# Kernel tuning notes

Measured on AMD Instinct MI355X. Metric: run time of the kernel, lower is better.

Reference implementation:

```python
import jax, jax.numpy as jnp
import numpy as np

N, E = 50000, 800000
IN, OUT, H, B = 512, 512, 8, 4  # num_bases=4, aggregators=['symnorm'] (PyG EGConv defaults)
FH = OUT // H  # per-head dim = 64
EPS = 1e-5


def setup_inputs() -> dict:
    key = jax.random.key(0)
    ks = jax.random.split(key, 8)
    s_in = 1.0 / np.sqrt(IN)
    return {
        "x": jax.random.normal(ks[0], (N, IN), jnp.float32),
        "edge_index": jax.random.randint(ks[1], (2, E), 0, N, jnp.int32),
        "W_bases": jax.random.normal(ks[2], (IN, B * FH), jnp.float32) * s_in,  # bases_lin (no bias)
        "W_comb": jax.random.normal(ks[3], (IN, H * B), jnp.float32) * s_in,    # comb_lin weight
        "b_comb": jnp.zeros((H * B,), jnp.float32),                               # comb_lin bias
        "conv_bias": jnp.zeros((OUT,), jnp.float32),                              # EGConv output bias
        "W_res": jax.random.normal(ks[4], (IN, OUT), jnp.float32) * s_in,        # res_connection
        "b_res": jnp.zeros((OUT,), jnp.float32),
        "gamma": jnp.ones((OUT,), jnp.float32),                                   # LayerNorm weight
        "beta": jnp.zeros((OUT,), jnp.float32),                                   # LayerNorm bias
    }


def reference(x, edge_index, W_bases, W_comb, b_comb, conv_bias, W_res, b_res, gamma, beta):
    n = x.shape[0]
    # --- gcn_norm with self-loops (symnorm aggregator) ---
    loops = jnp.arange(n, dtype=edge_index.dtype)
    src = jnp.concatenate([edge_index[0], loops])  # [E+N]
    dst = jnp.concatenate([edge_index[1], loops])
    deg = jax.ops.segment_sum(jnp.ones_like(src, dtype=x.dtype), dst, num_segments=n)
    dinv = jnp.where(deg > 0, jax.lax.rsqrt(jnp.maximum(deg, 1.0)), 0.0)
    norm = dinv[src] * dinv[dst]  # [E+N]

    # --- EGConv: bases projection, symnorm aggregation, per-head combination ---
    bases = x @ W_bases  # [N, B*FH]
    agg = jax.ops.segment_sum(bases[src] * norm[:, None], dst, num_segments=n)  # [N, B*FH]
    weightings = (x @ W_comb + b_comb).reshape(n, H, B)        # [N, H, B]  (num_aggrs=1)
    agg = agg.reshape(n, B, FH)                                  # [N, B, FH]
    conv_out = jnp.einsum('nhb,nbf->nhf', weightings, agg).reshape(n, OUT) + conv_bias

    # --- residual + LayerNorm + ReLU (dropout p=0 -> identity) ---
    out = conv_out + x @ W_res + b_res
    mu = out.mean(-1, keepdims=True)
    var = out.var(-1, keepdims=True)
    out = (out - mu) * jax.lax.rsqrt(var + EPS) * gamma + beta
    return jax.nn.relu(out)
```

## Files before the change

kernel.cpp:

```cpp
#include <hip/hip_runtime.h>
#include <hip/hip_bf16.h>

#define KDIM 512
#define ODIM 512
#define NB 4
#define NH 8
#define FH 64
#define BFH 256
#define HB 32
#define NCAT 896
#define COL_W 256
#define COL_R 288
#define LN_EPS 1e-5f
#define SCAN_BLK 1024

typedef __attribute__((ext_vector_type(8))) short short8;
typedef __attribute__((ext_vector_type(4))) float floatx4;

__device__ __forceinline__ float b2f(unsigned short u) {
    union { unsigned int i; float f; } v; v.i = ((unsigned int)u) << 16; return v.f;
}
__device__ __forceinline__ unsigned short f2b(float f) {
    __hip_bfloat16 h = __float2bfloat16(f);
    return *(unsigned short*)&h;
}
__device__ __forceinline__ void async16(const void* g, void* l) {
    __builtin_amdgcn_global_load_lds(
        (__attribute__((address_space(1))) unsigned int*)(g),
        (__attribute__((address_space(3))) unsigned int*)(l),
        16, 0, 0);
}

__global__ void deg_kernel(const int* __restrict__ dst, int* __restrict__ deg, int E) {
    int i = blockIdx.x * blockDim.x + threadIdx.x;
    if (i < E) atomicAdd(&deg[dst[i]], 1);
}

__global__ __launch_bounds__(256) void scan_sums_kernel(
        const int* __restrict__ deg, int* __restrict__ sums, int N) {
    int t = threadIdx.x;
    int idx = blockIdx.x * SCAN_BLK + t * 4;
    int4 v = {0, 0, 0, 0};
    if (idx + 3 < N) v = *(const int4*)(deg + idx);
    else {
        if (idx < N)     v.x = deg[idx];
        if (idx + 1 < N) v.y = deg[idx + 1];
        if (idx + 2 < N) v.z = deg[idx + 2];
        if (idx + 3 < N) v.w = deg[idx + 3];
    }
    int s = v.x + v.y + v.z + v.w;
    #pragma unroll
    for (int o = 32; o > 0; o >>= 1) s += __shfl_down(s, o, 64);
    __shared__ int ws[4];
    int lane = t & 63, w = t >> 6;
    if (lane == 0) ws[w] = s;
    __syncthreads();
    if (t == 0) sums[blockIdx.x] = ws[0] + ws[1] + ws[2] + ws[3];
}

__global__ __launch_bounds__(1024) void scan_base_kernel(
        int* __restrict__ sums, int nb) {
    __shared__ int sm[1024];
    int t = threadIdx.x;
    int own = (t < nb) ? sums[t] : 0;
    sm[t] = own;
    __syncthreads();
    for (int o = 1; o < 1024; o <<= 1) {
        int u = (t >= o) ? sm[t - o] : 0;
        __syncthreads();
        sm[t] += u;
        __syncthreads();
    }
    if (t < nb) sums[t] = sm[t] - own;
}

__global__ __launch_bounds__(256) void scan_write_kernel(
        const int* __restrict__ deg, const int* __restrict__ bases,
        int* __restrict__ offsets, int* __restrict__ woff,
        float* __restrict__ dinv, int N, int E) {
    int t = threadIdx.x;
    int idx = blockIdx.x * SCAN_BLK + t * 4;
    int4 v = {0, 0, 0, 0};
    if (idx + 3 < N) v = *(const int4*)(deg + idx);
    else {
        if (idx < N)     v.x = deg[idx];
        if (idx + 1 < N) v.y = deg[idx + 1];
        if (idx + 2 < N) v.z = deg[idx + 2];
        if (idx + 3 < N) v.w = deg[idx + 3];
    }
    int s = v.x + v.y + v.z + v.w;
    __shared__ int sm[256];
    sm[t] = s;
    __syncthreads();
    for (int o = 1; o < 256; o <<= 1) {
        int u = (t >= o) ? sm[t - o] : 0;
        __syncthreads();
        sm[t] += u;
        __syncthreads();
    }
    int o0 = sm[t] - s + bases[blockIdx.x];
    int o1 = o0 + v.x, o2 = o1 + v.y, o3 = o2 + v.z;
    if (idx + 3 < N) {
        int4 ov = {o0, o1, o2, o3};
        *(int4*)(offsets + idx) = ov;
        *(int4*)(woff + idx) = ov;
        float4 dv = {rsqrtf((float)v.x + 1.0f), rsqrtf((float)v.y + 1.0f),
                     rsqrtf((float)v.z + 1.0f), rsqrtf((float)v.w + 1.0f)};
        *(float4*)(dinv + idx) = dv;
    } else {
        int oo[4] = {o0, o1, o2, o3};
        int vv[4] = {v.x, v.y, v.z, v.w};
        for (int j = 0; j < 4; j++) {
            if (idx + j < N) {
                offsets[idx + j] = oo[j];
                woff[idx + j] = oo[j];
                dinv[idx + j] = rsqrtf((float)vv[j] + 1.0f);
            }
        }
    }
    if (blockIdx.x == 0 && t == 0) offsets[N] = E;
}

__global__ void fill_kernel(const int* __restrict__ src, const int* __restrict__ dst,
                            int* __restrict__ woff, int* __restrict__ ebuf, int E) {
    int i = blockIdx.x * blockDim.x + threadIdx.x;
    if (i < E) {
        int pos = atomicAdd(&woff[dst[i]], 1);
        ebuf[pos] = src[i];
    }
}

__global__ __launch_bounds__(256) void prep_kernel(
        const float* __restrict__ x, unsigned short* __restrict__ xb, long total4,
        int nCvtBlocks,
        const float* __restrict__ Wb, const float* __restrict__ Wc,
        const float* __restrict__ Wr, const float* __restrict__ bcomb,
        const float* __restrict__ bres,
        unsigned short* __restrict__ wT, float* __restrict__ bias_cat) {
    int blk = blockIdx.x;
    if (blk < nCvtBlocks) {
        long i = (long)blk * 256 + threadIdx.x;
        if (i >= total4) return;
        float4 v = ((const float4*)x)[i];
        ushort4 u;
        u.x = f2b(v.x); u.y = f2b(v.y); u.z = f2b(v.z); u.w = f2b(v.w);
        ((ushort4*)xb)[i] = u;
    } else {
        int idx = (blk - nCvtBlocks) * 256 + threadIdx.x;
        if (idx >= NCAT * KDIM) return;
        int c = idx >> 9, k = idx & (KDIM - 1);
        float v;
        if (c < BFH)                   v = Wb[(size_t)k * BFH + c];
        else if (c < COL_R)            v = Wc[(size_t)k * HB + (c - COL_W)];
        else if (c < COL_R + ODIM)     v = Wr[(size_t)k * ODIM + (c - COL_R)];
        else                           v = 0.0f;
        wT[(size_t)c * KDIM + k] = f2b(v);
        if (k == 0) {
            float bv = 0.0f;
            if (c >= COL_W && c < COL_R)             bv = bcomb[c - COL_W];
            else if (c >= COL_R && c < COL_R + ODIM) bv = bres[c - COL_R];
            bias_cat[c] = bv;
        }
    }
}

#define BM 128
#define BN 128
#define BK 32
#define SLD 136

__global__ __launch_bounds__(256) void mfma_gemm_kernel(
        const unsigned short* __restrict__ xb,
        const unsigned short* __restrict__ wT,
        const float* __restrict__ bias_cat,
        unsigned short* __restrict__ Cb,
        int N) {
    __shared__ short lds[8192];
    short* As = lds;
    short* Bs = lds + 4096;
    int t = threadIdx.x;
    int l = t & 63, w = t >> 6;
    int wr = w >> 1, wc = w & 1;
    int quad = l >> 4, m = l & 15;
    int row0 = blockIdx.y * BM;
    int col0 = blockIdx.x * BN;

    floatx4 acc[4][4];
    floatx4 zero4 = {0.f, 0.f, 0.f, 0.f};
    #pragma unroll
    for (int i = 0; i < 4; i++)
        #pragma unroll
        for (int j = 0; j < 4; j++) acc[i][j] = zero4;

    int ar0 = row0 + (w << 4) + (l >> 2);
    int ar1 = ar0 + 64;
    int brow = col0 + (w << 4) + (l >> 2);
    int kk = (l & 3) * 8;
    const unsigned short* agp0 = xb + (size_t)min(ar0, N - 1) * KDIM + kk;
    const unsigned short* agp1 = xb + (size_t)min(ar1, N - 1) * KDIM + kk;
    const unsigned short* bgp0 = wT + (size_t)brow * KDIM + kk;
    const unsigned short* bgp1 = bgp0 + (size_t)64 * KDIM;
    short* al0 = As + w * 512;
    short* al1 = As + 2048 + w * 512;
    short* bl0 = Bs + w * 512;
    short* bl1 = Bs + 2048 + w * 512;

    for (int k0 = 0; k0 < KDIM; k0 += BK) {
        __syncthreads();
        async16(agp0 + k0, al0);
        async16(agp1 + k0, al1);
        async16(bgp0 + k0, bl0);
        async16(bgp1 + k0, bl1);
        __syncthreads();

        short8 a[4], b[4];
        #pragma unroll
        for (int i = 0; i < 4; i++)
            a[i] = *(const short8*)(As + (wr * 64 + i * 16 + m) * BK + quad * 8);
        #pragma unroll
        for (int j = 0; j < 4; j++)
            b[j] = *(const short8*)(Bs + (wc * 64 + j * 16 + m) * BK + quad * 8);
        #pragma unroll
        for (int i = 0; i < 4; i++)
            #pragma unroll
            for (int j = 0; j < 4; j++)
                acc[i][j] = __builtin_amdgcn_mfma_f32_16x16x32_bf16(
                    a[i], b[j], acc[i][j], 0, 0, 0);
    }

    float bj[4];
    #pragma unroll
    for (int j = 0; j < 4; j++) bj[j] = bias_cat[col0 + wc * 64 + j * 16 + m];

    unsigned short* stage = (unsigned short*)lds;
    #pragma unroll
    for (int i = 0; i < 4; i++) {
        __syncthreads();
        #pragma unroll
        for (int j = 0; j < 4; j++)
            #pragma unroll
            for (int r = 0; r < 4; r++)
                stage[(wr * 16 + quad * 4 + r) * SLD + wc * 64 + j * 16 + m] =
                    f2b(acc[i][j][r] + bj[j]);
        __syncthreads();
        #pragma unroll
        for (int u = t; u < 512; u += 256) {
            int lr = u >> 4, c8 = u & 15;
            int gr = row0 + ((lr & 16) ? 64 : 0) + i * 16 + (lr & 15);
            if (gr < N) {
                int4 v = *(const int4*)(stage + lr * SLD + c8 * 8);
                *(int4*)(Cb + (size_t)gr * NCAT + col0 + c8 * 8) = v;
            }
        }
    }
}

__global__ __launch_bounds__(256) void gather_kernel(
        const int* __restrict__ offsets, const int* __restrict__ ebuf,
        const float* __restrict__ dinv, const unsigned short* __restrict__ Cb,
        unsigned short* __restrict__ agg, int N) {
    int wave = (blockIdx.x * blockDim.x + threadIdx.x) >> 6;
    int lane = threadIdx.x & 63;
    if (wave >= N) return;
    int n = wave;
    float di = dinv[n];
    float self = di * di;
    ushort4 u = ((const ushort4*)(Cb + (size_t)n * NCAT))[lane];
    float ax = b2f(u.x) * self, ay = b2f(u.y) * self;
    float az = b2f(u.z) * self, aw = b2f(u.w) * self;
    int e = offsets[n], end = offsets[n + 1];
    for (; e + 1 < end; e += 2) {
        int s0 = ebuf[e], s1 = ebuf[e + 1];
        float n0 = dinv[s0] * di, n1 = dinv[s1] * di;
        ushort4 u0 = ((const ushort4*)(Cb + (size_t)s0 * NCAT))[lane];
        ushort4 u1 = ((const ushort4*)(Cb + (size_t)s1 * NCAT))[lane];
        ax += b2f(u0.x) * n0 + b2f(u1.x) * n1;
        ay += b2f(u0.y) * n0 + b2f(u1.y) * n1;
        az += b2f(u0.z) * n0 + b2f(u1.z) * n1;
        aw += b2f(u0.w) * n0 + b2f(u1.w) * n1;
    }
    if (e < end) {
        int s0 = ebuf[e];
        float n0 = dinv[s0] * di;
        ushort4 u0 = ((const ushort4*)(Cb + (size_t)s0 * NCAT))[lane];
        ax += b2f(u0.x) * n0; ay += b2f(u0.y) * n0;
        az += b2f(u0.z) * n0; aw += b2f(u0.w) * n0;
    }
    ushort4 r;
    r.x = f2b(ax); r.y = f2b(ay); r.z = f2b(az); r.w = f2b(aw);
    ((ushort4*)(agg + (size_t)n * BFH))[lane] = r;
}

__global__ __launch_bounds__(256) void combine_kernel(
        const unsigned short* __restrict__ agg, const unsigned short* __restrict__ Cb,
        const float* __restrict__ conv_bias, const float* __restrict__ gamma,
        const float* __restrict__ beta, float* __restrict__ out, int N) {
    int wave = (blockIdx.x * blockDim.x + threadIdx.x) >> 6;
    if (wave >= N) return;
    int lane = threadIdx.x & 63;
    int n = wave;
    int h = lane >> 3;
    int f0 = (lane & 7) * 8;
    int t0 = lane * 8;

    const unsigned short* crow = Cb + (size_t)n * NCAT;
    ushort4 wu = *(const ushort4*)(crow + COL_W + h * 4);
    float w0 = b2f(wu.x), w1 = b2f(wu.y), w2 = b2f(wu.z), w3 = b2f(wu.w);

    const unsigned short* arow = agg + (size_t)n * BFH;
    short8 a0 = *(const short8*)(arow + 0 * FH + f0);
    short8 a1 = *(const short8*)(arow + 1 * FH + f0);
    short8 a2 = *(const short8*)(arow + 2 * FH + f0);
    short8 a3 = *(const short8*)(arow + 3 * FH + f0);

    short8 rv = *(const short8*)(crow + COL_R + t0);

    float4 cb0 = *(const float4*)(conv_bias + t0);
    float4 cb1 = *(const float4*)(conv_bias + t0 + 4);
    float cb[8] = {cb0.x, cb0.y, cb0.z, cb0.w, cb1.x, cb1.y, cb1.z, cb1.w};

    float v[8];
    float s = 0.f, s2 = 0.f;
    #pragma unroll
    for (int j = 0; j < 8; j++) {
        float conv = w0 * b2f((unsigned short)a0[j]) + w1 * b2f((unsigned short)a1[j])
                   + w2 * b2f((unsigned short)a2[j]) + w3 * b2f((unsigned short)a3[j]);
        float val = conv + cb[j] + b2f((unsigned short)rv[j]);
        v[j] = val;
        s += val;
        s2 += val * val;
    }
    #pragma unroll
    for (int o = 32; o > 0; o >>= 1) {
        s  += __shfl_xor(s, o, 64);
        s2 += __shfl_xor(s2, o, 64);
    }
    float mu = s * (1.0f / (float)ODIM);
    float var = s2 * (1.0f / (float)ODIM) - mu * mu;
    float rstd = rsqrtf(var + LN_EPS);

    float4 g0 = *(const float4*)(gamma + t0);
    float4 g1 = *(const float4*)(gamma + t0 + 4);
    float4 be0 = *(const float4*)(beta + t0);
    float4 be1 = *(const float4*)(beta + t0 + 4);
    float g[8] = {g0.x, g0.y, g0.z, g0.w, g1.x, g1.y, g1.z, g1.w};
    float be[8] = {be0.x, be0.y, be0.z, be0.w, be1.x, be1.y, be1.z, be1.w};

    float ov[8];
    #pragma unroll
    for (int j = 0; j < 8; j++) {
        float o = (v[j] - mu) * rstd * g[j] + be[j];
        ov[j] = fmaxf(o, 0.0f);
    }
    float4* op = (float4*)(out + (size_t)n * ODIM + t0);
    op[0] = make_float4(ov[0], ov[1], ov[2], ov[3]);
    op[1] = make_float4(ov[4], ov[5], ov[6], ov[7]);
}

static inline char* ws_alloc(char*& p, size_t bytes) {
    char* r = p;
    p += (bytes + 255) & ~(size_t)255;
    return r;
}

extern "C" void kernel_launch(void* const* d_in, const int* in_sizes, int n_in,
                              void* d_out, int out_size, void* d_ws, size_t ws_size,
                              hipStream_t stream) {
    const float* x         = (const float*)d_in[0];
    const int*   ei        = (const int*)d_in[1];
    const float* W_bases   = (const float*)d_in[2];
    const float* W_comb    = (const float*)d_in[3];
    const float* b_comb    = (const float*)d_in[4];
    const float* conv_bias = (const float*)d_in[5];
    const float* W_res     = (const float*)d_in[6];
    const float* b_res     = (const float*)d_in[7];
    const float* gamma     = (const float*)d_in[8];
    const float* beta      = (const float*)d_in[9];

    int N = in_sizes[0] / KDIM;
    int E = in_sizes[1] / 2;
    const int* src = ei;
    const int* dst = ei + E;
    int nScanBlocks = (N + SCAN_BLK - 1) / SCAN_BLK;

    char* p = (char*)d_ws;
    int*   deg      = (int*)ws_alloc(p, sizeof(int) * (size_t)N);
    int*   offsets  = (int*)ws_alloc(p, sizeof(int) * (size_t)(N + 1));
    int*   woff     = (int*)ws_alloc(p, sizeof(int) * (size_t)N);
    int*   ebuf     = (int*)ws_alloc(p, sizeof(int) * (size_t)E);
    int*   sums     = (int*)ws_alloc(p, sizeof(int) * (size_t)nScanBlocks);
    float* dinv     = (float*)ws_alloc(p, sizeof(float) * (size_t)N);
    float* bias_cat = (float*)ws_alloc(p, sizeof(float) * NCAT);
    unsigned short* agg = (unsigned short*)ws_alloc(p, 2ull * N * BFH);
    unsigned short* Cb  = (unsigned short*)ws_alloc(p, 2ull * N * NCAT);
    unsigned short* xb  = (unsigned short*)ws_alloc(p, 2ull * N * KDIM);
    unsigned short* wT  = (unsigned short*)ws_alloc(p, 2ull * NCAT * KDIM);
    float* out = (float*)d_out;

    hipMemsetAsync(deg, 0, sizeof(int) * (size_t)N, stream);

    long total4 = (long)N * KDIM / 4;
    int nCvtBlocks = (int)((total4 + 255) / 256);
    int nStageBlocks = (NCAT * KDIM + 255) / 256;
    prep_kernel<<<nCvtBlocks + nStageBlocks, 256, 0, stream>>>(
        x, xb, total4, nCvtBlocks, W_bases, W_comb, W_res, b_comb, b_res,
        wT, bias_cat);

    deg_kernel<<<(E + 255) / 256, 256, 0, stream>>>(dst, deg, E);
    scan_sums_kernel<<<nScanBlocks, 256, 0, stream>>>(deg, sums, N);
    scan_base_kernel<<<1, 1024, 0, stream>>>(sums, nScanBlocks);
    scan_write_kernel<<<nScanBlocks, 256, 0, stream>>>(deg, sums, offsets, woff,
                                                       dinv, N, E);
    fill_kernel<<<(E + 255) / 256, 256, 0, stream>>>(src, dst, woff, ebuf, E);

    dim3 gg(NCAT / BN, (N + BM - 1) / BM);
    mfma_gemm_kernel<<<gg, 256, 0, stream>>>(xb, wT, bias_cat, Cb, N);

    gather_kernel<<<(N + 3) / 4, 256, 0, stream>>>(offsets, ebuf, dinv, Cb, agg, N);
    combine_kernel<<<(N + 3) / 4, 256, 0, stream>>>(agg, Cb, conv_bias, gamma,
                                                    beta, out, N);
}
```

Baseline: 467.9 us.

## Double-buffer GEMM LDS tiles and remap workgroups for XCD-aware L2 locality

Result: faster. 443.2 us (-5.3%).

```diff
diff --git a/kernel.cpp b/kernel.cpp
--- a/kernel.cpp
+++ b/kernel.cpp
@@ -175,15 +175,25 @@
         const float* __restrict__ bias_cat,
         unsigned short* __restrict__ Cb,
         int N) {
-    __shared__ short lds[8192];
-    short* As = lds;
-    short* Bs = lds + 4096;
+    __shared__ short lds[16384];
+    short* As0 = lds;
+    short* Bs0 = lds + 4096;
+    short* As1 = lds + 8192;
+    short* Bs1 = lds + 12288;
     int t = threadIdx.x;
     int l = t & 63, w = t >> 6;
     int wr = w >> 1, wc = w & 1;
     int quad = l >> 4, m = l & 15;
-    int row0 = blockIdx.y * BM;
-    int col0 = blockIdx.x * BN;
+
+    int nwg = gridDim.x;
+    int orig = blockIdx.x;
+    int q = nwg >> 3, r = nwg & 7;
+    int xcd = orig & 7, slot = orig >> 3;
+    int wg = (xcd < r) ? (xcd * (q + 1) + slot)
+                       : (r * (q + 1) + (xcd - r) * q + slot);
+    int bx = wg % 7, by = wg / 7;
+    int row0 = by * BM;
+    int col0 = bx * BN;
 
     floatx4 acc[4][4];
     floatx4 zero4 = {0.f, 0.f, 0.f, 0.f};
@@ -200,19 +210,14 @@
     const unsigned short* agp1 = xb + (size_t)min(ar1, N - 1) * KDIM + kk;
     const unsigned short* bgp0 = wT + (size_t)brow * KDIM + kk;
     const unsigned short* bgp1 = bgp0 + (size_t)64 * KDIM;
-    short* al0 = As + w * 512;
-    short* al1 = As + 2048 + w * 512;
-    short* bl0 = Bs + w * 512;
-    short* bl1 = Bs + 2048 + w * 512;
-
-    for (int k0 = 0; k0 < KDIM; k0 += BK) {
-        __syncthreads();
-        async16(agp0 + k0, al0);
-        async16(agp1 + k0, al1);
-        async16(bgp0 + k0, bl0);
-        async16(bgp1 + k0, bl1);
-        __syncthreads();
-
+
+    auto stage = [&](short* A, short* B, int k0) {
+        async16(agp0 + k0, A + w * 512);
+        async16(agp1 + k0, A + 2048 + w * 512);
+        async16(bgp0 + k0, B + w * 512);
+        async16(bgp1 + k0, B + 2048 + w * 512);
+    };
+    auto compute = [&](const short* As, const short* Bs) {
         short8 a[4], b[4];
         #pragma unroll
         for (int i = 0; i < 4; i++)
@@ -226,29 +231,41 @@
             for (int j = 0; j < 4; j++)
                 acc[i][j] = __builtin_amdgcn_mfma_f32_16x16x32_bf16(
                     a[i], b[j], acc[i][j], 0, 0, 0);
+    };
+
+    stage(As0, Bs0, 0);
+    __syncthreads();
+
+    for (int k0 = 0; k0 < KDIM; k0 += 2 * BK) {
+        if (k0 + BK < KDIM) stage(As1, Bs1, k0 + BK);
+        compute(As0, Bs0);
+        __syncthreads();
+        if (k0 + 2 * BK < KDIM) stage(As0, Bs0, k0 + 2 * BK);
+        compute(As1, Bs1);
+        __syncthreads();
     }
 
     float bj[4];
     #pragma unroll
     for (int j = 0; j < 4; j++) bj[j] = bias_cat[col0 + wc * 64 + j * 16 + m];
 
-    unsigned short* stage = (unsigned short*)lds;
+    unsigned short* stage_buf = (unsigned short*)lds;
     #pragma unroll
     for (int i = 0; i < 4; i++) {
         __syncthreads();
         #pragma unroll
         for (int j = 0; j < 4; j++)
             #pragma unroll
-            for (int r = 0; r < 4; r++)
-                stage[(wr * 16 + quad * 4 + r) * SLD + wc * 64 + j * 16 + m] =
-                    f2b(acc[i][j][r] + bj[j]);
+            for (int r2 = 0; r2 < 4; r2++)
+                stage_buf[(wr * 16 + quad * 4 + r2) * SLD + wc * 64 + j * 16 + m] =
+                    f2b(acc[i][j][r2] + bj[j]);
         __syncthreads();
         #pragma unroll
         for (int u = t; u < 512; u += 256) {
             int lr = u >> 4, c8 = u & 15;
             int gr = row0 + ((lr & 16) ? 64 : 0) + i * 16 + (lr & 15);
             if (gr < N) {
-                int4 v = *(const int4*)(stage + lr * SLD + c8 * 8);
+                int4 v = *(const int4*)(stage_buf + lr * SLD + c8 * 8);
                 *(int4*)(Cb + (size_t)gr * NCAT + col0 + c8 * 8) = v;
             }
         }
@@ -413,8 +430,8 @@
                                                        dinv, N, E);
     fill_kernel<<<(E + 255) / 256, 256, 0, stream>>>(src, dst, woff, ebuf, E);
 
-    dim3 gg(NCAT / BN, (N + BM - 1) / BM);
-    mfma_gemm_kernel<<<gg, 256, 0, stream>>>(xb, wT, bias_cat, Cb, N);
+    int nYB = (N + BM - 1) / BM;
+    mfma_gemm_kernel<<<7 * nYB, 256, 0, stream>>>(xb, wT, bias_cat, Cb, N);
 
     gather_kernel<<<(N + 3) / 4, 256, 0, stream>>>(offsets, ebuf, dinv, Cb, agg, N);
     combine_kernel<<<(N + 3) / 4, 256, 0, stream>>>(agg, Cb, conv_bias, gamma,
```
